# Optimization experiments

Measured on AMD Instinct MI355X. Metric: run time of the kernel, lower is better.

Reference implementation:

```python
import jax, jax.numpy as jnp
import numpy as np

B, H, W = 16, 32, 64
HID, VOCAB, ENC_C, EMB = 256, 5000, 1024, 256


def _conv3x3(x, w, b):
    # x: [B,C,H,W], w: [O,I,3,3]
    y = jax.lax.conv_general_dilated(x, w, (1, 1), 'SAME',
                                     dimension_numbers=('NCHW', 'OIHW', 'NCHW'))
    return y + b[None, :, None, None]


def _gru(x, h, w_ih, w_hh, b_ih, b_hh):
    # torch GRUCell: gates ordered r, z, n
    gi = x @ w_ih.T + b_ih
    gh = h @ w_hh.T + b_hh
    ir, iz, inn = jnp.split(gi, 3, axis=1)
    hr, hz, hn = jnp.split(gh, 3, axis=1)
    r = jax.nn.sigmoid(ir + hr)
    z = jax.nn.sigmoid(iz + hz)
    n = jnp.tanh(inn + r * hn)
    return (1.0 - z) * n + z * h


def setup_inputs() -> dict:
    key = jax.random.key(0)
    ks = jax.random.split(key, 48)
    g = lambda i, shape, s=0.02: jax.random.normal(ks[i], shape, jnp.float32) * s
    inp = {
        'input_a': jax.random.randint(ks[0], (B,), 0, VOCAB),
        'input_hidden': jax.random.normal(ks[1], (B, 1, HID), jnp.float32),
        'encoder_outputs': jax.random.normal(ks[2], (B, ENC_C, H, W), jnp.float32),
        'attention_sum': jnp.zeros((B, 1, H, W), jnp.float32),
        'decoder_attention': jnp.zeros((B, 1, H, W), jnp.float32),
        'h_mask': jax.random.randint(ks[3], (B,), 1, H + 1),
        'w_mask': jax.random.randint(ks[4], (B,), 1, W + 1),
        'feature_w': W, 'feature_h': H, 'batch_size': B, 'gpu': 0,
        # parameters
        'emb_w': g(5, (VOCAB, EMB)),
        'gru1_w_ih': g(6, (3 * HID, EMB)), 'gru1_w_hh': g(7, (3 * HID, HID)),
        'gru1_b_ih': jnp.zeros((3 * HID,)), 'gru1_b_hh': jnp.zeros((3 * HID,)),
        'fc1_w': g(8, (256, HID)), 'fc1_b': jnp.zeros((256,)),
        'gru2_w_ih': g(9, (3 * HID, ENC_C)), 'gru2_w_hh': g(10, (3 * HID, HID)),
        'gru2_b_ih': jnp.zeros((3 * HID,)), 'gru2_b_hh': jnp.zeros((3 * HID,)),
        'out_w': g(11, (VOCAB, 128)), 'out_b': jnp.zeros((VOCAB,)),
        'emb2_w': g(12, (128, 256)), 'emb2_b': jnp.zeros((128,)),
        'conv1_w': g(13, (1, 1, 3, 3)), 'conv1_b': jnp.zeros((1,)),
        'convtan_w': g(14, (256, 256, 3, 3)), 'convtan_b': jnp.zeros((256,)),
        'fc2_w': g(15, (128, HID)), 'fc2_b': jnp.zeros((128,)),
        'ua_w': g(16, (256, ENC_C)), 'ua_b': jnp.zeros((256,)),
        'uf_w': g(17, (256, 1)), 'uf_b': jnp.zeros((256,)),
        'v_w': g(18, (1, 256)), 'v_b': jnp.zeros((1,)),
        'wc_w': g(19, (128, ENC_C)), 'wc_b': jnp.zeros((128,)),
        'bn1_g': jnp.ones((256,)), 'bn1_b': jnp.zeros((256,)),
        'bn1_rm': jnp.zeros((256,)), 'bn1_rv': jnp.ones((256,)),
    }
    return inp


def reference(input_a, input_hidden, encoder_outputs, feature_w, attention_sum,
              decoder_attention, feature_h, batch_size, h_mask, w_mask, gpu,
              emb_w, gru1_w_ih, gru1_w_hh, gru1_b_ih, gru1_b_hh, fc1_w, fc1_b,
              gru2_w_ih, gru2_w_hh, gru2_b_ih, gru2_b_hh, out_w, out_b,
              emb2_w, emb2_b, conv1_w, conv1_b, convtan_w, convtan_b,
              fc2_w, fc2_b, ua_w, ua_b, uf_w, uf_b, v_w, v_b, wc_w, wc_b,
              bn1_g, bn1_b, bn1_rm, bn1_rv):
    # vectorized mask construction (replaces per-batch python loop)
    mask = ((jnp.arange(feature_h)[None, :, None] < h_mask[:, None, None]) &
            (jnp.arange(feature_w)[None, None, :] < w_mask[:, None, None])
            ).astype(jnp.float32)  # [B,H,W]

    emb = emb_w[input_a]                                   # [B,256] (dropout=eval id)
    h0 = input_hidden.reshape(batch_size, HID)
    st = _gru(emb, h0, gru1_w_ih, gru1_w_hh, gru1_b_ih, gru1_b_hh)  # [B,HID]
    hidden1 = (st @ fc1_w.T + fc1_b)[:, None, None, :]     # [B,1,1,256]

    enc_t = jnp.transpose(encoder_outputs, (0, 2, 3, 1))   # [B,H,W,1024]
    dec_att = _conv3x3(decoder_attention, conv1_w, conv1_b)
    att_sum = attention_sum + dec_att                      # [B,1,H,W]
    att_t = jnp.transpose(att_sum, (0, 2, 3, 1))           # [B,H,W,1]

    enc1 = enc_t @ ua_w.T + ua_b                           # [B,H,W,256]
    att1 = att_t @ uf_w.T + uf_b                           # [B,H,W,256]
    et = hidden1 + enc1 + att1

    et_c = jnp.transpose(et, (0, 3, 1, 2))                 # [B,256,H,W]
    et_c = _conv3x3(et_c, convtan_w, convtan_b)
    et_c = et_c * mask[:, None]
    inv_std = (bn1_g / jnp.sqrt(bn1_rv + 1e-5))[None, :, None, None]
    et_c = (et_c - bn1_rm[None, :, None, None]) * inv_std + bn1_b[None, :, None, None]
    et_c = jnp.tanh(et_c)
    et_hw = jnp.transpose(et_c, (0, 2, 3, 1))              # [B,H,W,256]

    e = (et_hw @ v_w.T + v_b)[..., 0]                      # [B,H,W]
    e_exp = jnp.exp(e) * mask
    e_sum = e_exp.sum((1, 2))                              # [B]
    alpha = e_exp / (e_sum[:, None, None] + 1e-8)
    alpha4 = alpha[:, None]                                # [B,1,H,W]

    ct = (alpha4 * encoder_outputs).sum((2, 3))            # [B,1024]
    h2 = _gru(ct, st, gru2_w_ih, gru2_w_hh, gru2_b_ih, gru2_b_hh)
    hidden_next = h2[:, None, :]                           # [B,1,HID]

    pre = (h2 @ fc2_w.T + fc2_b) + (emb @ emb2_w.T + emb2_b) + (ct @ wc_w.T + wc_b)
    output = jax.nn.log_softmax(pre @ out_w.T + out_b, axis=1)[:, None, :]  # [B,1,V]
    return (output, hidden_next, alpha4, att_sum)
```

## Files before the change

### kernel.cpp

```cpp
#include <hip/hip_runtime.h>
#include <hip/hip_bf16.h>

#define HH 32
#define WW 64
#define HWSZ 2048
#define ENC 1024
#define VOCAB 5000

typedef __attribute__((ext_vector_type(8))) short short8;
typedef __attribute__((ext_vector_type(4))) short short4v;
typedef __attribute__((ext_vector_type(4))) float f32x4;

#if defined(__has_builtin)
#if __has_builtin(__builtin_amdgcn_global_load_lds)
#define HAVE_GLD_LDS 1
#endif
#endif

__device__ __forceinline__ float sigm(float x) { return 1.0f / (1.0f + expf(-x)); }

__device__ __forceinline__ unsigned short f2bf(float x) {
    unsigned u = __float_as_uint(x);
    unsigned r = (u + 0x7fff + ((u >> 16) & 1)) >> 16;
    return (unsigned short)r;
}

#ifdef HAVE_GLD_LDS
__device__ __forceinline__ void gld_lds16(const unsigned short* g, unsigned short* l) {
    __builtin_amdgcn_global_load_lds(
        (const __attribute__((address_space(1))) void*)g,
        (__attribute__((address_space(3))) void*)l,
        16, 0, 0);
}
#endif

template <int NI>
__device__ __forceinline__ float dotk(const float* __restrict__ w,
                                      const float* __restrict__ x, int l) {
    float s = 0.f;
    #pragma unroll
    for (int i = 0; i < NI; ++i) {
        f32x4 wv = *(const f32x4*)(w + i * 64 + l * 4);
        f32x4 xv = *(const f32x4*)(x + i * 64 + l * 4);
        s += wv.x * xv.x + wv.y * xv.y + wv.z * xv.z + wv.w * xv.w;
    }
    return s;
}
__device__ __forceinline__ float red16(float s) {
    s += __shfl_xor(s, 1, 64);
    s += __shfl_xor(s, 2, 64);
    s += __shfl_xor(s, 4, 64);
    s += __shfl_xor(s, 8, 64);
    return s;
}

__global__ __launch_bounds__(256) void k_prep(
    const float* __restrict__ ua_w, unsigned short* __restrict__ ub,
    const float* __restrict__ cw, unsigned short* __restrict__ wr,
    const float* __restrict__ att_in, const float* __restrict__ dec,
    const float* __restrict__ c1w, const float* __restrict__ c1b,
    float* __restrict__ out_attsum,
    const float* __restrict__ wb, const float* __restrict__ g,
    const float* __restrict__ bb, const float* __restrict__ rm,
    const float* __restrict__ rv, float* __restrict__ cs, float* __restrict__ csh,
    const int* __restrict__ input_a, const float* __restrict__ input_hidden,
    const float* __restrict__ emb_w,
    const float* __restrict__ w_ih, const float* __restrict__ w_hh,
    const float* __restrict__ b_ih, const float* __restrict__ b_hh,
    float* __restrict__ gi, float* __restrict__ gh,
    float* __restrict__ e_zero,
    const int* __restrict__ h_mask, const int* __restrict__ w_mask,
    int* __restrict__ wl_cnt, int* __restrict__ wl_conv, int* __restrict__ wl_et)
{
    int blk = blockIdx.x, t = threadIdx.x;
    if (blk < 1024) {
        int idx = blk * 256 + t;
        ub[idx] = f2bf(ua_w[idx]);
    } else if (blk < 1280) {
        int idx = (blk - 1024) * 256 + t;
        const float* p = cw + (size_t)idx * 9;
        #pragma unroll
        for (int k = 0; k < 9; ++k) wr[k * 65536 + idx] = f2bf(p[k]);
    } else if (blk < 1408) {
        int idx = (blk - 1280) * 256 + t;
        int b = idx >> 11, hw = idx & 2047;
        int h = hw >> 6, w = hw & 63;
        float s = c1b[0];
        #pragma unroll
        for (int dy = 0; dy < 3; ++dy) {
            int hh = h + dy - 1;
            if ((unsigned)hh < (unsigned)HH) {
                #pragma unroll
                for (int dx = 0; dx < 3; ++dx) {
                    int wi = w + dx - 1;
                    if ((unsigned)wi < (unsigned)WW)
                        s += dec[b * HWSZ + hh * WW + wi] * c1w[dy * 3 + dx];
                }
            }
        }
        out_attsum[idx] = att_in[idx] + s;
    } else if (blk == 1408) {
        int c = t;
        float s = g[c] * rsqrtf(rv[c] + 1e-5f);
        cs[c] = s;
        csh[c] = (wb[c] - rm[c]) * s + bb[c];
    } else if (blk < 2177) {
        int gid = (blk - 1409) * 256 + t;
        int o = gid >> 4, l = gid & 15;
        int j = o >> 4, b = o & 15;
        int ia = input_a[b];
        float si = dotk<4>(w_ih + (size_t)j * 256, emb_w + (size_t)ia * 256, l);
        float sh = dotk<4>(w_hh + (size_t)j * 256, input_hidden + b * 256, l);
        si = red16(si); sh = red16(sh);
        if (l == 0) {
            gi[j * 16 + b] = si + b_ih[j];
            gh[j * 16 + b] = sh + b_hh[j];
        }
    } else if (blk < 2305) {
        e_zero[(blk - 2177) * 256 + t] = 0.f;
    } else {
        __shared__ int s_hm[16], s_wm[16], s_oc[16], s_oe[16];
        if (t < 16) { s_hm[t] = h_mask[t]; s_wm[t] = w_mask[t]; }
        __syncthreads();
        if (t == 0) {
            int oc = 0, oe = 0;
            for (int b = 0; b < 16; ++b) {
                s_oc[b] = oc; oc += s_hm[b];
                int nr = min(s_hm[b] + 1, 32);
                int nw = 1 + (s_wm[b] >= 32 ? 1 : 0);
                s_oe[b] = oe; oe += nr * nw;
            }
            wl_cnt[0] = oc;
            wl_cnt[1] = oe;
        }
        __syncthreads();
        for (int idx = t; idx < 512; idx += 256) {
            int b = idx >> 5, h = idx & 31;
            if (h < s_hm[b]) wl_conv[s_oc[b] + h] = (b << 5) | h;
        }
        for (int idx = t; idx < 1024; idx += 256) {
            int b = idx >> 6, bx = idx & 63;
            int row = bx >> 1, wh = bx & 1;
            int nr = min(s_hm[b] + 1, 32);
            int nw = 1 + (s_wm[b] >= 32 ? 1 : 0);
            if (row < nr && wh < nw)
                wl_et[s_oe[b] + row * nw + wh] = (b << 6) | bx;
        }
    }
}

__global__ __launch_bounds__(256) void k_frontbc(
    const int* __restrict__ input_a, const float* __restrict__ emb_w,
    const float* __restrict__ input_hidden,
    const float* __restrict__ gi, const float* __restrict__ gh,
    const float* __restrict__ fc1_w, const float* __restrict__ fc1_b,
    const float* __restrict__ ua_b, const float* __restrict__ uf_b,
    float* __restrict__ st, float* __restrict__ embv, float* __restrict__ addc)
{
    __shared__ float st_s[256];
    int b = blockIdx.x, i = threadIdx.x;
    float r = sigm(gi[i * 16 + b] + gh[i * 16 + b]);
    float z = sigm(gi[(256 + i) * 16 + b] + gh[(256 + i) * 16 + b]);
    float n = tanhf(gi[(512 + i) * 16 + b] + r * gh[(512 + i) * 16 + b]);
    float h0 = input_hidden[b * 256 + i];
    float v = (1.f - z) * n + z * h0;
    st_s[i] = v;
    st[b * 256 + i] = v;
    embv[b * 256 + i] = emb_w[(size_t)input_a[b] * 256 + i];
    __syncthreads();
    int c = i;
    const float* w = fc1_w + (size_t)c * 256;
    float acc = 0.f;
    for (int k = 0; k < 256; ++k) acc += st_s[k] * w[k];
    addc[b * 256 + c] = acc + fc1_b[c] + ua_b[c] + uf_b[c];
}

__global__ __launch_bounds__(256) void k_et(
    const float* __restrict__ enc, const unsigned short* __restrict__ ua_bf,
    const float* __restrict__ addc, const float* __restrict__ uf_w,
    const float* __restrict__ attsum,
    const int* __restrict__ wl_cnt, const int* __restrict__ wl_et,
    unsigned short* __restrict__ et)
{
    __shared__ __align__(16) unsigned short As[256 * 64];
    __shared__ __align__(16) unsigned short Bs[32 * 64];
    int id = blockIdx.x;
    if (id >= wl_cnt[1]) return;
    int ent = wl_et[id];
    int b = ent >> 6, bx = ent & 63;
    int hw0 = bx * 32;
    int t = threadIdx.x;
    int wv = t >> 6;
    int l15 = t & 15, quad = (t >> 4) & 3;
    int xb = l15 & 7;
    f32x4 acc[4][2];
    #pragma unroll
    for (int i = 0; i < 4; ++i)
        #pragma unroll
        for (int j = 0; j < 2; ++j) acc[i][j] = (f32x4)0.f;

    int p = t & 31, g3 = t >> 5;
    const float* encb = enc + (size_t)b * ENC * HWSZ + hw0 + p;

    float pfv[8];
    {
        const float* ep = encb + (size_t)(g3 * 8) * HWSZ;
        #pragma unroll
        for (int j = 0; j < 8; ++j) pfv[j] = ep[(size_t)j * HWSZ];
    }

    for (int k0 = 0; k0 < ENC; k0 += 64) {
        short8 bv;
        #pragma unroll
        for (int j = 0; j < 8; ++j) bv[j] = (short)f2bf(pfv[j]);
        if (k0 + 64 < ENC) {
            const float* ep = encb + (size_t)(k0 + 64 + g3 * 8) * HWSZ;
            #pragma unroll
            for (int j = 0; j < 8; ++j) pfv[j] = ep[(size_t)j * HWSZ];
        }
        __syncthreads();

        #pragma unroll
        for (int i = 0; i < 8; ++i) {
            int s = t + 256 * i;
            int c = s >> 3, kq = s & 7;
            const unsigned short* src =
                ua_bf + (size_t)c * ENC + k0 + ((kq ^ (c & 7)) << 3);
#ifdef HAVE_GLD_LDS
            gld_lds16(src, As + (size_t)(wv * 64 + 256 * i) * 8);
#else
            *(uint4*)(As + (size_t)s * 8) = *(const uint4*)src;
#endif
        }
        *(short8*)(Bs + p * 64 + ((g3 ^ (p & 7)) << 3)) = bv;
        __syncthreads();

        #pragma unroll
        for (int kk = 0; kk < 2; ++kk) {
            short8 af[4], bfr[2];
            #pragma unroll
            for (int mt = 0; mt < 4; ++mt) {
                int c = wv * 64 + mt * 16 + l15;
                af[mt] = *(const short8*)(As + c * 64 + (((kk * 4 + quad) ^ xb) << 3));
            }
            #pragma unroll
            for (int nt = 0; nt < 2; ++nt) {
                int n = nt * 16 + l15;
                bfr[nt] = *(const short8*)(Bs + n * 64 + (((kk * 4 + quad) ^ xb) << 3));
            }
            #pragma unroll
            for (int mt = 0; mt < 4; ++mt)
                #pragma unroll
                for (int nt = 0; nt < 2; ++nt)
                    acc[mt][nt] = __builtin_amdgcn_mfma_f32_16x16x32_bf16(
                        af[mt], bfr[nt], acc[mt][nt], 0, 0, 0);
        }
    }
    float at[2];
    #pragma unroll
    for (int nt = 0; nt < 2; ++nt) at[nt] = attsum[b * HWSZ + hw0 + nt * 16 + l15];
    #pragma unroll
    for (int mt = 0; mt < 4; ++mt) {
        int cb = wv * 64 + mt * 16 + quad * 4;
        float ad[4], uw[4];
        #pragma unroll
        for (int r = 0; r < 4; ++r) { ad[r] = addc[b * 256 + cb + r]; uw[r] = uf_w[cb + r]; }
        #pragma unroll
        for (int nt = 0; nt < 2; ++nt) {
            ushort4 pk;
            pk.x = f2bf(acc[mt][nt][0] + ad[0] + at[nt] * uw[0]);
            pk.y = f2bf(acc[mt][nt][1] + ad[1] + at[nt] * uw[1]);
            pk.z = f2bf(acc[mt][nt][2] + ad[2] + at[nt] * uw[2]);
            pk.w = f2bf(acc[mt][nt][3] + ad[3] + at[nt] * uw[3]);
            *(ushort4*)(et + (size_t)(b * HWSZ + hw0 + nt * 16 + l15) * 256 + cb) = pk;
        }
    }
}

__global__ __launch_bounds__(256) void k_conv(
    const unsigned short* __restrict__ et, const unsigned short* __restrict__ wr,
    const float* __restrict__ cs, const float* __restrict__ csh,
    const float* __restrict__ v_w,
    const int* __restrict__ wl_cnt, const int* __restrict__ wl_conv,
    const int* __restrict__ w_mask,
    float* __restrict__ e_out)
{
    __shared__ unsigned short Ls[66 * 264];
    __shared__ float red[64][17];
    int id = blockIdx.x;
    if (id >= 2 * wl_cnt[0]) return;
    int ent = wl_conv[id >> 1];
    int b = ent >> 5, h = ent & 31;
    int c0 = (id & 1) * 128;
    int t = threadIdx.x;
    int wm = w_mask[b];
    int ntmax = (wm + 15) >> 4;
    int pxmax = ntmax * 16 + 2;
    int wv = t >> 6, l15 = t & 15, quad = (t >> 4) & 3;
    f32x4 acc[2][4];
    #pragma unroll
    for (int i = 0; i < 2; ++i)
        #pragma unroll
        for (int j = 0; j < 4; ++j) acc[i][j] = (f32x4)0.f;

    for (int dy = 0; dy < 3; ++dy) {
        int hr = h + dy - 1;
        if ((unsigned)hr >= (unsigned)HH) continue;
        __syncthreads();
        const unsigned short* rowp = et + (size_t)(b * HH + hr) * WW * 256;
        for (int idx = t; idx < pxmax * 32; idx += 256) {
            int p = idx >> 5, s = idx & 31;
            short8 v;
            if (p == 0 || p == 65) v = (short8)0;
            else v = *(const short8*)(rowp + (p - 1) * 256 + s * 8);
            *(short8*)(Ls + p * 264 + s * 8) = v;
        }
        __syncthreads();
        for (int dx = 0; dx < 3; ++dx) {
            int tap = dy * 3 + dx;
            const unsigned short* wrt = wr + (size_t)tap * 65536;
            #pragma unroll
            for (int kc = 0; kc < 8; ++kc) {
                short8 af[2], bfr[4];
                #pragma unroll
                for (int mt = 0; mt < 2; ++mt)
                    af[mt] = *(const short8*)(wrt +
                        (size_t)(c0 + wv * 32 + mt * 16 + l15) * 256 + kc * 32 + quad * 8);
                #pragma unroll
                for (int nt = 0; nt < 4; ++nt) {
                    if (nt < ntmax) {
                        int wrow = nt * 16 + l15 + dx;
                        bfr[nt] = *(const short8*)(Ls + wrow * 264 + kc * 32 + quad * 8);
                    }
                }
                #pragma unroll
                for (int mt = 0; mt < 2; ++mt)
                    #pragma unroll
                    for (int nt = 0; nt < 4; ++nt)
                        if (nt < ntmax)
                            acc[mt][nt] = __builtin_amdgcn_mfma_f32_16x16x32_bf16(
                                af[mt], bfr[nt], acc[mt][nt], 0, 0, 0);
            }
        }
    }
    float p[4] = {0.f, 0.f, 0.f, 0.f};
    #pragma unroll
    for (int mt = 0; mt < 2; ++mt) {
        int cb = c0 + wv * 32 + mt * 16 + quad * 4;
        #pragma unroll
        for (int r = 0; r < 4; ++r) {
            float sc = cs[cb + r], sh = csh[cb + r], vw = v_w[cb + r];
            #pragma unroll
            for (int nt = 0; nt < 4; ++nt) {
                if (nt < ntmax) {
                    float x = acc[mt][nt][r] * sc + sh;
                    p[nt] += tanhf(x) * vw;
                }
            }
        }
    }
    __syncthreads();
    #pragma unroll
    for (int nt = 0; nt < 4; ++nt) red[nt * 16 + l15][wv * 4 + quad] = p[nt];
    __syncthreads();
    if (t < 64) {
        float s = 0.f;
        #pragma unroll
        for (int i = 0; i < 16; ++i) s += red[t][i];
        atomicAdd(&e_out[(b * HH + h) * WW + t], s);
    }
}

__global__ __launch_bounds__(256) void k_ctalpha(
    const float* __restrict__ enc, const float* __restrict__ e_acc,
    const float* __restrict__ v_b,
    const int* __restrict__ h_mask, const int* __restrict__ w_mask,
    float* __restrict__ alpha_out, float* __restrict__ ct)
{
    __shared__ float a_s[HWSZ];
    __shared__ float rbuf[4];
    int b = blockIdx.y, cg = blockIdx.x, t = threadIdx.x;
    int hm = h_mask[b], wm = w_mask[b];
    float vb = v_b[0];
    float vals[8];
    float psum = 0.f;
    #pragma unroll
    for (int u = 0; u < 8; ++u) {
        int s = u * 256 + t;
        int h = s >> 6, w = s & 63;
        float e = e_acc[b * HWSZ + s] + vb;
        float ex = (h < hm && w < wm) ? expf(e) : 0.f;
        vals[u] = ex;
        psum += ex;
    }
    for (int off = 1; off < 64; off <<= 1) psum += __shfl_xor(psum, off, 64);
    if ((t & 63) == 0) rbuf[t >> 6] = psum;
    __syncthreads();
    float inv = 1.f / (rbuf[0] + rbuf[1] + rbuf[2] + rbuf[3] + 1e-8f);
    #pragma unroll
    for (int u = 0; u < 8; ++u) {
        int s = u * 256 + t;
        float a = vals[u] * inv;
        a_s[s] = a;
        if (cg == 0) alpha_out[b * HWSZ + s] = a;
    }
    __syncthreads();
    int wave = t >> 6, lane = t & 63;
    int c = cg * 4 + wave;
    const float* ep = enc + ((size_t)(b * ENC + c)) * HWSZ;
    float s = 0.f;
    int imax = hm * 64;
    for (int i = lane; i < imax; i += 64) s += ep[i] * a_s[i];
    for (int off = 32; off; off >>= 1) s += __shfl_down(s, off, 64);
    if (lane == 0) ct[b * ENC + c] = s;
}

__global__ __launch_bounds__(256) void k_gru2a(
    const float* __restrict__ ct, const float* __restrict__ st,
    const float* __restrict__ w_ih, const float* __restrict__ w_hh,
    const float* __restrict__ b_ih, const float* __restrict__ b_hh,
    float* __restrict__ gi, float* __restrict__ gh)
{
    int gid = blockIdx.x * 256 + threadIdx.x;
    int o = gid >> 4, l = gid & 15;
    int j = o >> 4, b = o & 15;
    float si = dotk<16>(w_ih + (size_t)j * ENC, ct + b * ENC, l);
    float sh = dotk<4>(w_hh + (size_t)j * 256, st + b * 256, l);
    si = red16(si); sh = red16(sh);
    if (l == 0) {
        gi[j * 16 + b] = si + b_ih[j];
        gh[j * 16 + b] = sh + b_hh[j];
    }
}

__global__ __launch_bounds__(256) void k_gates2(
    const float* __restrict__ st, const float* __restrict__ gi,
    const float* __restrict__ gh, float* __restrict__ h2,
    float* __restrict__ out_hidden)
{
    int b = blockIdx.x, i = threadIdx.x;
    float r = sigm(gi[i * 16 + b] + gh[i * 16 + b]);
    float z = sigm(gi[(256 + i) * 16 + b] + gh[(256 + i) * 16 + b]);
    float n = tanhf(gi[(512 + i) * 16 + b] + r * gh[(512 + i) * 16 + b]);
    float v = (1.f - z) * n + z * st[b * 256 + i];
    h2[b * 256 + i] = v;
    out_hidden[b * 256 + i] = v;
}

__global__ __launch_bounds__(256) void k_pre(
    const float* __restrict__ h2, const float* __restrict__ emb,
    const float* __restrict__ ct,
    const float* __restrict__ fc2_w, const float* __restrict__ fc2_b,
    const float* __restrict__ emb2_w, const float* __restrict__ emb2_b,
    const float* __restrict__ wc_w, const float* __restrict__ wc_b,
    float* __restrict__ pre)
{
    int gid = blockIdx.x * 256 + threadIdx.x;
    int o = gid >> 4, l = gid & 15;
    int j = o >> 4, b = o & 15;
    float s = dotk<4>(fc2_w + (size_t)j * 256, h2 + b * 256, l)
            + dotk<4>(emb2_w + (size_t)j * 256, emb + b * 256, l)
            + dotk<16>(wc_w + (size_t)j * ENC, ct + b * ENC, l);
    s = red16(s);
    if (l == 0) pre[b * 128 + j] = s + fc2_b[j] + emb2_b[j] + wc_b[j];
}

__global__ __launch_bounds__(256) void k_logits(
    const float* __restrict__ pre, const float* __restrict__ out_w,
    const float* __restrict__ out_b, float* __restrict__ logits)
{
    int gid = blockIdx.x * 256 + threadIdx.x;
    int o = gid >> 4, l = gid & 15;
    int j = o >> 4, b = o & 15;
    float s = dotk<2>(out_w + (size_t)j * 128, pre + b * 128, l);
    s = red16(s);
    if (l == 0) logits[b * VOCAB + j] = s + out_b[j];
}

__global__ __launch_bounds__(256) void k_lsm(
    const float* __restrict__ logits, float* __restrict__ out)
{
    __shared__ float buf[VOCAB];
    __shared__ float rbuf[4];
    int b = blockIdx.x, t = threadIdx.x;
    float mx = -1e30f;
    for (int s = t; s < VOCAB; s += 256) {
        float v = logits[b * VOCAB + s];
        buf[s] = v;
        mx = fmaxf(mx, v);
    }
    for (int off = 1; off < 64; off <<= 1) mx = fmaxf(mx, __shfl_xor(mx, off, 64));
    if ((t & 63) == 0) rbuf[t >> 6] = mx;
    __syncthreads();
    mx = fmaxf(fmaxf(rbuf[0], rbuf[1]), fmaxf(rbuf[2], rbuf[3]));
    __syncthreads();
    float se = 0.f;
    for (int s = t; s < VOCAB; s += 256) se += expf(buf[s] - mx);
    for (int off = 1; off < 64; off <<= 1) se += __shfl_xor(se, off, 64);
    if ((t & 63) == 0) rbuf[t >> 6] = se;
    __syncthreads();
    float lse = mx + logf(rbuf[0] + rbuf[1] + rbuf[2] + rbuf[3]);
    for (int s = t; s < VOCAB; s += 256) out[b * VOCAB + s] = buf[s] - lse;
}

extern "C" void kernel_launch(void* const* d_in, const int* in_sizes, int n_in,
                              void* d_out, int out_size, void* d_ws, size_t ws_size,
                              hipStream_t stream)
{
    const int*   input_a      = (const int*)d_in[0];
    const float* input_hidden = (const float*)d_in[1];
    const float* enc          = (const float*)d_in[2];
    const float* att_in       = (const float*)d_in[3];
    const float* dec_att      = (const float*)d_in[4];
    const int*   h_mask       = (const int*)d_in[5];
    const int*   w_mask       = (const int*)d_in[6];
    const float* emb_w        = (const float*)d_in[11];
    const float* g1_wih       = (const float*)d_in[12];
    const float* g1_whh       = (const float*)d_in[13];
    const float* g1_bih       = (const float*)d_in[14];
    const float* g1_bhh       = (const float*)d_in[15];
    const float* fc1_w        = (const float*)d_in[16];
    const float* fc1_b        = (const float*)d_in[17];
    const float* g2_wih       = (const float*)d_in[18];
    const float* g2_whh       = (const float*)d_in[19];
    const float* g2_bih       = (const float*)d_in[20];
    const float* g2_bhh       = (const float*)d_in[21];
    const float* out_w        = (const float*)d_in[22];
    const float* out_b        = (const float*)d_in[23];
    const float* emb2_w       = (const float*)d_in[24];
    const float* emb2_b       = (const float*)d_in[25];
    const float* c1w          = (const float*)d_in[26];
    const float* c1b          = (const float*)d_in[27];
    const float* ctw          = (const float*)d_in[28];
    const float* ctb          = (const float*)d_in[29];
    const float* fc2_w        = (const float*)d_in[30];
    const float* fc2_b        = (const float*)d_in[31];
    const float* ua_w         = (const float*)d_in[32];
    const float* ua_b         = (const float*)d_in[33];
    const float* uf_w         = (const float*)d_in[34];
    const float* uf_b         = (const float*)d_in[35];
    const float* v_w          = (const float*)d_in[36];
    const float* v_b          = (const float*)d_in[37];
    const float* wc_w         = (const float*)d_in[38];
    const float* wc_b         = (const float*)d_in[39];
    const float* bn_g         = (const float*)d_in[40];
    const float* bn_b         = (const float*)d_in[41];
    const float* bn_rm        = (const float*)d_in[42];
    const float* bn_rv        = (const float*)d_in[43];

    float* out        = (float*)d_out;
    float* out_logits = out;
    float* out_hidden = out + 80000;
    float* out_alpha  = out + 84096;
    float* out_attsum = out + 116864;

    char* ws = (char*)d_ws;
    unsigned short* et_t  = (unsigned short*)ws;
    unsigned short* ua_bf = (unsigned short*)(ws + 16777216);
    unsigned short* w_r   = (unsigned short*)(ws + 17301504);
    float* f      = (float*)(ws + 18481152);
    float* st     = f;
    float* embv   = f + 4096;
    float* addc   = f + 8192;
    float* e_ws   = f + 12288;
    float* ct     = f + 45056;
    float* h2     = f + 61440;
    float* pre    = f + 65536;
    float* logits = f + 67584;
    float* gi1    = f + 147584;
    float* gh1    = f + 159872;
    float* gi2    = f + 172160;
    float* gh2    = f + 184448;
    float* cs     = f + 196736;
    float* csh    = f + 196992;
    int*   wl_cnt  = (int*)(f + 197248);
    int*   wl_conv = wl_cnt + 2;
    int*   wl_et   = wl_cnt + 514;

    k_prep<<<2306, 256, 0, stream>>>(ua_w, ua_bf, ctw, w_r,
                                     att_in, dec_att, c1w, c1b, out_attsum,
                                     ctb, bn_g, bn_b, bn_rm, bn_rv, cs, csh,
                                     input_a, input_hidden, emb_w,
                                     g1_wih, g1_whh, g1_bih, g1_bhh, gi1, gh1,
                                     e_ws, h_mask, w_mask,
                                     wl_cnt, wl_conv, wl_et);
    k_frontbc<<<16, 256, 0, stream>>>(input_a, emb_w, input_hidden, gi1, gh1,
                                      fc1_w, fc1_b, ua_b, uf_b, st, embv, addc);

    k_et<<<1024, 256, 0, stream>>>(enc, ua_bf, addc, uf_w, out_attsum,
                                   wl_cnt, wl_et, et_t);
    k_conv<<<1024, 256, 0, stream>>>(et_t, w_r, cs, csh, v_w,
                                     wl_cnt, wl_conv, w_mask, e_ws);

    k_ctalpha<<<dim3(256, 16), 256, 0, stream>>>(enc, e_ws, v_b, h_mask, w_mask,
                                                 out_alpha, ct);
    k_gru2a<<<768, 256, 0, stream>>>(ct, st, g2_wih, g2_whh, g2_bih, g2_bhh, gi2, gh2);
    k_gates2<<<16, 256, 0, stream>>>(st, gi2, gh2, h2, out_hidden);
    k_pre<<<128, 256, 0, stream>>>(h2, embv, ct, fc2_w, fc2_b, emb2_w, emb2_b,
                                   wc_w, wc_b, pre);
    k_logits<<<5000, 256, 0, stream>>>(pre, out_w, out_b, logits);
    k_lsm<<<16, 256, 0, stream>>>(logits, out_logits);
}
```

Before: 413.3 us.

## Split et and conv kernels over channel halves/quarters; fuse pre projection into gates

Result: slower. 482.0 us (+16.6%).

```diff
diff --git a/kernel.cpp b/kernel.cpp
--- a/kernel.cpp
+++ b/kernel.cpp
@@ -182,20 +182,21 @@
     const int* __restrict__ wl_cnt, const int* __restrict__ wl_et,
     unsigned short* __restrict__ et)
 {
-    __shared__ __align__(16) unsigned short As[256 * 64];
+    __shared__ __align__(16) unsigned short As[128 * 64];
     __shared__ __align__(16) unsigned short Bs[32 * 64];
     int id = blockIdx.x;
-    if (id >= wl_cnt[1]) return;
-    int ent = wl_et[id];
+    if (id >= 2 * wl_cnt[1]) return;
+    int ent = wl_et[id >> 1];
+    int c0 = (id & 1) * 128;
     int b = ent >> 6, bx = ent & 63;
     int hw0 = bx * 32;
     int t = threadIdx.x;
     int wv = t >> 6;
     int l15 = t & 15, quad = (t >> 4) & 3;
     int xb = l15 & 7;
-    f32x4 acc[4][2];
-    #pragma unroll
-    for (int i = 0; i < 4; ++i)
+    f32x4 acc[2][2];
+    #pragma unroll
+    for (int i = 0; i < 2; ++i)
         #pragma unroll
         for (int j = 0; j < 2; ++j) acc[i][j] = (f32x4)0.f;
 
@@ -221,11 +222,11 @@
         __syncthreads();
 
         #pragma unroll
-        for (int i = 0; i < 8; ++i) {
+        for (int i = 0; i < 4; ++i) {
             int s = t + 256 * i;
             int c = s >> 3, kq = s & 7;
             const unsigned short* src =
-                ua_bf + (size_t)c * ENC + k0 + ((kq ^ (c & 7)) << 3);
+                ua_bf + (size_t)(c0 + c) * ENC + k0 + ((kq ^ (c & 7)) << 3);
 #ifdef HAVE_GLD_LDS
             gld_lds16(src, As + (size_t)(wv * 64 + 256 * i) * 8);
 #else
@@ -237,10 +238,10 @@
 
         #pragma unroll
         for (int kk = 0; kk < 2; ++kk) {
-            short8 af[4], bfr[2];
+            short8 af[2], bfr[2];
             #pragma unroll
-            for (int mt = 0; mt < 4; ++mt) {
-                int c = wv * 64 + mt * 16 + l15;
+            for (int mt = 0; mt < 2; ++mt) {
+                int c = wv * 32 + mt * 16 + l15;
                 af[mt] = *(const short8*)(As + c * 64 + (((kk * 4 + quad) ^ xb) << 3));
             }
             #pragma unroll
@@ -249,7 +250,7 @@
                 bfr[nt] = *(const short8*)(Bs + n * 64 + (((kk * 4 + quad) ^ xb) << 3));
             }
             #pragma unroll
-            for (int mt = 0; mt < 4; ++mt)
+            for (int mt = 0; mt < 2; ++mt)
                 #pragma unroll
                 for (int nt = 0; nt < 2; ++nt)
                     acc[mt][nt] = __builtin_amdgcn_mfma_f32_16x16x32_bf16(
@@ -260,8 +261,8 @@
     #pragma unroll
     for (int nt = 0; nt < 2; ++nt) at[nt] = attsum[b * HWSZ + hw0 + nt * 16 + l15];
     #pragma unroll
-    for (int mt = 0; mt < 4; ++mt) {
-        int cb = wv * 64 + mt * 16 + quad * 4;
+    for (int mt = 0; mt < 2; ++mt) {
+        int cb = c0 + wv * 32 + mt * 16 + quad * 4;
         float ad[4], uw[4];
         #pragma unroll
         for (int r = 0; r < 4; ++r) { ad[r] = addc[b * 256 + cb + r]; uw[r] = uf_w[cb + r]; }
@@ -288,20 +289,18 @@
     __shared__ unsigned short Ls[66 * 264];
     __shared__ float red[64][17];
     int id = blockIdx.x;
-    if (id >= 2 * wl_cnt[0]) return;
-    int ent = wl_conv[id >> 1];
+    if (id >= 4 * wl_cnt[0]) return;
+    int ent = wl_conv[id >> 2];
     int b = ent >> 5, h = ent & 31;
-    int c0 = (id & 1) * 128;
+    int c0 = (id & 3) * 64;
     int t = threadIdx.x;
     int wm = w_mask[b];
     int ntmax = (wm + 15) >> 4;
     int pxmax = ntmax * 16 + 2;
     int wv = t >> 6, l15 = t & 15, quad = (t >> 4) & 3;
-    f32x4 acc[2][4];
-    #pragma unroll
-    for (int i = 0; i < 2; ++i)
-        #pragma unroll
-        for (int j = 0; j < 4; ++j) acc[i][j] = (f32x4)0.f;
+    f32x4 acc[4];
+    #pragma unroll
+    for (int j = 0; j < 4; ++j) acc[j] = (f32x4)0.f;
 
     for (int dy = 0; dy < 3; ++dy) {
         int hr = h + dy - 1;
@@ -321,11 +320,9 @@
             const unsigned short* wrt = wr + (size_t)tap * 65536;
             #pragma unroll
             for (int kc = 0; kc < 8; ++kc) {
-                short8 af[2], bfr[4];
-                #pragma unroll
-                for (int mt = 0; mt < 2; ++mt)
-                    af[mt] = *(const short8*)(wrt +
-                        (size_t)(c0 + wv * 32 + mt * 16 + l15) * 256 + kc * 32 + quad * 8);
+                short8 af, bfr[4];
+                af = *(const short8*)(wrt +
+                    (size_t)(c0 + wv * 16 + l15) * 256 + kc * 32 + quad * 8);
                 #pragma unroll
                 for (int nt = 0; nt < 4; ++nt) {
                     if (nt < ntmax) {
@@ -334,26 +331,23 @@
                     }
                 }
                 #pragma unroll
-                for (int mt = 0; mt < 2; ++mt)
-                    #pragma unroll
-                    for (int nt = 0; nt < 4; ++nt)
-                        if (nt < ntmax)
-                            acc[mt][nt] = __builtin_amdgcn_mfma_f32_16x16x32_bf16(
-                                af[mt], bfr[nt], acc[mt][nt], 0, 0, 0);
+                for (int nt = 0; nt < 4; ++nt)
+                    if (nt < ntmax)
+                        acc[nt] = __builtin_amdgcn_mfma_f32_16x16x32_bf16(
+                            af, bfr[nt], acc[nt], 0, 0, 0);
             }
         }
     }
     float p[4] = {0.f, 0.f, 0.f, 0.f};
-    #pragma unroll
-    for (int mt = 0; mt < 2; ++mt) {
-        int cb = c0 + wv * 32 + mt * 16 + quad * 4;
+    {
+        int cb = c0 + wv * 16 + quad * 4;
         #pragma unroll
         for (int r = 0; r < 4; ++r) {
             float sc = cs[cb + r], sh = csh[cb + r], vw = v_w[cb + r];
             #pragma unroll
             for (int nt = 0; nt < 4; ++nt) {
                 if (nt < ntmax) {
-                    float x = acc[mt][nt][r] * sc + sh;
+                    float x = acc[nt][r] * sc + sh;
                     p[nt] += tanhf(x) * vw;
                 }
             }
@@ -435,34 +429,50 @@
 
 __global__ __launch_bounds__(256) void k_gates2(
     const float* __restrict__ st, const float* __restrict__ gi,
-    const float* __restrict__ gh, float* __restrict__ h2,
-    float* __restrict__ out_hidden)
-{
+    const float* __restrict__ gh, const float* __restrict__ embv,
+    const float* __restrict__ ct,
+    const float* __restrict__ fc2_w, const float* __restrict__ fc2_b,
+    const float* __restrict__ emb2_w, const float* __restrict__ emb2_b,
+    const float* __restrict__ wc_w, const float* __restrict__ wc_b,
+    float* __restrict__ h2, float* __restrict__ out_hidden,
+    float* __restrict__ pre)
+{
+    __shared__ float h2_s[256];
     int b = blockIdx.x, i = threadIdx.x;
     float r = sigm(gi[i * 16 + b] + gh[i * 16 + b]);
     float z = sigm(gi[(256 + i) * 16 + b] + gh[(256 + i) * 16 + b]);
     float n = tanhf(gi[(512 + i) * 16 + b] + r * gh[(512 + i) * 16 + b]);
     float v = (1.f - z) * n + z * st[b * 256 + i];
+    h2_s[i] = v;
     h2[b * 256 + i] = v;
     out_hidden[b * 256 + i] = v;
-}
-
-__global__ __launch_bounds__(256) void k_pre(
-    const float* __restrict__ h2, const float* __restrict__ emb,
-    const float* __restrict__ ct,
-    const float* __restrict__ fc2_w, const float* __restrict__ fc2_b,
-    const float* __restrict__ emb2_w, const float* __restrict__ emb2_b,
-    const float* __restrict__ wc_w, const float* __restrict__ wc_b,
-    float* __restrict__ pre)
-{
-    int gid = blockIdx.x * 256 + threadIdx.x;
-    int o = gid >> 4, l = gid & 15;
-    int j = o >> 4, b = o & 15;
-    float s = dotk<4>(fc2_w + (size_t)j * 256, h2 + b * 256, l)
-            + dotk<4>(emb2_w + (size_t)j * 256, emb + b * 256, l)
-            + dotk<16>(wc_w + (size_t)j * ENC, ct + b * ENC, l);
-    s = red16(s);
-    if (l == 0) pre[b * 128 + j] = s + fc2_b[j] + emb2_b[j] + wc_b[j];
+    __syncthreads();
+    if (i < 128) {
+        int j = i;
+        float s = fc2_b[j] + emb2_b[j] + wc_b[j];
+        const float* wf = fc2_w + (size_t)j * 256;
+        const float* we = emb2_w + (size_t)j * 256;
+        const float* wc = wc_w + (size_t)j * ENC;
+        const float* em = embv + b * 256;
+        const float* cb = ct + b * ENC;
+        float a0 = 0.f, a1 = 0.f, a2 = 0.f;
+        #pragma unroll 8
+        for (int k = 0; k < 64; ++k) {
+            f32x4 w0 = *(const f32x4*)(wf + k * 4);
+            a0 += w0.x * h2_s[k * 4] + w0.y * h2_s[k * 4 + 1]
+                + w0.z * h2_s[k * 4 + 2] + w0.w * h2_s[k * 4 + 3];
+            f32x4 w1 = *(const f32x4*)(we + k * 4);
+            f32x4 e1 = *(const f32x4*)(em + k * 4);
+            a1 += w1.x * e1.x + w1.y * e1.y + w1.z * e1.z + w1.w * e1.w;
+        }
+        #pragma unroll 8
+        for (int k = 0; k < 256; ++k) {
+            f32x4 w2 = *(const f32x4*)(wc + k * 4);
+            f32x4 c2 = *(const f32x4*)(cb + k * 4);
+            a2 += w2.x * c2.x + w2.y * c2.y + w2.z * c2.z + w2.w * c2.w;
+        }
+        pre[b * 128 + j] = s + a0 + a1 + a2;
+    }
 }
 
 __global__ __launch_bounds__(256) void k_logits(
@@ -587,17 +597,17 @@
     k_frontbc<<<16, 256, 0, stream>>>(input_a, emb_w, input_hidden, gi1, gh1,
                                       fc1_w, fc1_b, ua_b, uf_b, st, embv, addc);
 
-    k_et<<<1024, 256, 0, stream>>>(enc, ua_bf, addc, uf_w, out_attsum,
+    k_et<<<2048, 256, 0, stream>>>(enc, ua_bf, addc, uf_w, out_attsum,
                                    wl_cnt, wl_et, et_t);
-    k_conv<<<1024, 256, 0, stream>>>(et_t, w_r, cs, csh, v_w,
+    k_conv<<<2048, 256, 0, stream>>>(et_t, w_r, cs, csh, v_w,
                                      wl_cnt, wl_conv, w_mask, e_ws);
 
     k_ctalpha<<<dim3(256, 16), 256, 0, stream>>>(enc, e_ws, v_b, h_mask, w_mask,
                                                  out_alpha, ct);
     k_gru2a<<<768, 256, 0, stream>>>(ct, st, g2_wih, g2_whh, g2_bih, g2_bhh, gi2, gh2);
-    k_gates2<<<16, 256, 0, stream>>>(st, gi2, gh2, h2, out_hidden);
-    k_pre<<<128, 256, 0, stream>>>(h2, embv, ct, fc2_w, fc2_b, emb2_w, emb2_b,
-                                   wc_w, wc_b, pre);
+    k_gates2<<<16, 256, 0, stream>>>(st, gi2, gh2, embv, ct,
+                                     fc2_w, fc2_b, emb2_w, emb2_b, wc_w, wc_b,
+                                     h2, out_hidden, pre);
     k_logits<<<5000, 256, 0, stream>>>(pre, out_w, out_b, logits);
     k_lsm<<<16, 256, 0, stream>>>(logits, out_logits);
 }
```
